# Kernel optimization log

Hardware: AMD Instinct MI355X
Metric: run time of the kernel (lower is better)

## Reference

```python
import jax, jax.numpy as jnp
import numpy as np

S = 3000    # number of candidate spans (rows of g_i)
P = 80000   # total (mention, antecedent) pairs
GI = 768    # gi_dim
DD = 20     # distance/genre/speaker embedding dim
HID = 150   # mlp hidden dim (fixed in source)
ORDER = 2   # N: one higher-order refinement pass


def setup_inputs() -> dict:
    key = jax.random.key(0)
    ks = jax.random.split(key, 18)
    gij = 3 * GI + 3 * DD
    g_i = jax.random.normal(ks[0], (S, GI), jnp.float32)
    mention_scores = jax.random.normal(ks[1], (S, 1), jnp.float32)
    # sorted segment ids: ragged antecedent counts per mention, grouped contiguously
    mention_ids = jnp.sort(jax.random.randint(ks[2], (P,), 0, S, dtype=jnp.int32))
    antecedent_ids = jax.random.randint(ks[3], (P,), 0, S, dtype=jnp.int32)
    dist_bins = jax.random.randint(ks[4], (P,), 0, 10, dtype=jnp.int32)
    genre_ids = jax.random.randint(ks[5], (P,), 0, 7, dtype=jnp.int32) + 1   # 1..7, 0 is padding_idx
    speaker_ids = jax.random.randint(ks[6], (P,), 0, 2, dtype=jnp.int32) + 1  # 1..2, 0 is padding_idx
    w = lambda k, shp: 0.02 * jax.random.normal(k, shp, jnp.float32)
    dist_emb = w(ks[7], (10, DD))
    genre_emb = w(ks[8], (8, DD)).at[0].set(0.0)     # padding_idx=0
    speaker_emb = w(ks[9], (3, DD)).at[0].set(0.0)   # padding_idx=0
    W1 = w(ks[10], (gij, HID)); b1 = jnp.zeros((HID,), jnp.float32)
    W2 = w(ks[11], (HID, HID)); b2 = jnp.zeros((HID,), jnp.float32)
    W3 = w(ks[12], (HID, 1)); b3 = jnp.zeros((1,), jnp.float32)
    Wf = w(ks[13], (2 * GI, 1)); bf = jnp.zeros((1,), jnp.float32)
    return {"g_i": g_i, "mention_scores": mention_scores, "mention_ids": mention_ids,
            "antecedent_ids": antecedent_ids, "dist_bins": dist_bins, "genre_ids": genre_ids,
            "speaker_ids": speaker_ids, "dist_emb": dist_emb, "genre_emb": genre_emb,
            "speaker_emb": speaker_emb, "W1": W1, "b1": b1, "W2": W2, "b2": b2,
            "W3": W3, "b3": b3, "Wf": Wf, "bf": bf}


def _mlp(x, W1, b1, W2, b2, W3, b3):
    h = jax.nn.relu(x @ W1 + b1)
    h = jax.nn.relu(h @ W2 + b2)
    return h @ W3 + b3


def reference(g_i, mention_scores, mention_ids, antecedent_ids, dist_bins, genre_ids,
              speaker_ids, dist_emb, genre_emb, speaker_emb, W1, b1, W2, b2, W3, b3, Wf, bf):
    phi = jnp.concatenate([dist_emb[dist_bins], genre_emb[genre_ids], speaker_emb[speaker_ids]], axis=1)  # [P,60]
    seg = dict(num_segments=S, indices_are_sorted=True)
    g = g_i
    scores = None
    for n in range(ORDER):
        i_g = g[mention_ids]                # [P,GI] gather
        j_g = g[antecedent_ids]             # [P,GI] gather
        pairs = jnp.concatenate([i_g, j_g, i_g * j_g, phi], axis=1)  # [P,gij]
        scores = _mlp(pairs, W1, b1, W2, b2, W3, b3)                 # [P,1]
        if n < ORDER - 1:
            # higher_order_refinement: ragged segment softmax + weighted scatter update
            s = scores[:, 0]
            seg_max = jax.ops.segment_max(s, mention_ids, **seg)
            safe_max = jnp.where(jnp.isfinite(seg_max), seg_max, 0.0)
            e = jnp.exp(s - safe_max[mention_ids])
            denom = jax.ops.segment_sum(e, mention_ids, **seg)
            attn = e / jnp.where(denom > 0, denom, 1.0)[mention_ids]
            weighted = jax.ops.segment_sum(attn[:, None] * j_g, mention_ids, **seg)  # [S,GI]
            counts = jax.ops.segment_sum(jnp.ones_like(s), mention_ids, **seg)
            f = jax.nn.sigmoid(jnp.concatenate([g, weighted], axis=1) @ Wf + bf)  # [S,1]
            # NOTE: faithful to the source bug: f * mention_id (the integer index), not f * mention_g
            ids_f = jnp.arange(S, dtype=g.dtype)[:, None]
            g_new = f * ids_f + (1.0 - f) * weighted
            g = jnp.where(counts[:, None] > 0, g_new, g)
    s_i = mention_scores[mention_ids]
    s_j = mention_scores[antecedent_ids]
    coref_scores = s_i + s_j + scores       # [P,1]
    # segment softmax with an extra epsilon (score 0) logit per mention
    c = coref_scores[:, 0]
    seg_max = jax.ops.segment_max(c, mention_ids, **seg)
    m = jnp.maximum(jnp.where(jnp.isfinite(seg_max), seg_max, 0.0), 0.0)  # include epsilon logit 0
    e = jnp.exp(c - m[mention_ids])
    denom = jax.ops.segment_sum(e, mention_ids, **seg) + jnp.exp(-m)
    pair_probs = e / denom[mention_ids]     # [P]
    eps_probs = jnp.exp(-m) / denom         # [S]
    return coref_scores, pair_probs, eps_probs
```

## Files before the change

### kernel.cpp

```cpp
#include <hip/hip_runtime.h>

#define GI   768
#define HID  150
#define HPAD 160
#define DDIM 20

typedef __attribute__((ext_vector_type(8))) short v8s;
typedef __attribute__((ext_vector_type(4))) float f32x4;
typedef __attribute__((ext_vector_type(16))) float f32x16;

#define MFMA(A, B, C)   __builtin_amdgcn_mfma_f32_32x32x16_bf16(A, B, C, 0, 0, 0)
#define MFMA16(A, B, C) __builtin_amdgcn_mfma_f32_16x16x32_bf16(A, B, C, 0, 0, 0)

__device__ __forceinline__ ushort bf16rn(float x) {
  unsigned u = __float_as_uint(x);
  return (ushort)((u + 0x7fffu + ((u >> 16) & 1u)) >> 16);
}
__device__ __forceinline__ void tsplit(float x, ushort& h, ushort& l) {
  unsigned u = __float_as_uint(x);
  h = (ushort)(u >> 16);
  float d = x - __uint_as_float(u & 0xffff0000u);
  l = (ushort)(__float_as_uint(d) >> 16);
}
__device__ __forceinline__ uint4 pack8(const ushort* v) {
  uint4 r;
  r.x = v[0] | ((unsigned)v[1] << 16); r.y = v[2] | ((unsigned)v[3] << 16);
  r.z = v[4] | ((unsigned)v[5] << 16); r.w = v[6] | ((unsigned)v[7] << 16);
  return r;
}
__device__ __forceinline__ v8s mk8(const ushort* v) {
  union { uint4 u; v8s s; } t;
  t.u = pack8(v);
  return t.s;
}

__global__ void seg_kernel(const int* __restrict__ mI, int* __restrict__ segs,
                           int P, int S) {
  int m = blockIdx.x * 256 + threadIdx.x;
  if (m > S) return;
  int lo = 0, hi = P;
  while (lo < hi) { int mid = (lo + hi) >> 1; if (mI[mid] < m) lo = mid + 1; else hi = mid; }
  segs[m] = lo;
}

__global__ void phi_kernel(const float* __restrict__ de, const float* __restrict__ ge,
                           const float* __restrict__ se, const float* __restrict__ W1,
                           float* __restrict__ phiW) {
  int idx = blockIdx.x * 256 + threadIdx.x;
  if (idx >= 21 * HPAD) return;
  int row = idx / HPAD, h = idx % HPAD;
  float v = 0.f;
  if (h < HID) {
    const float* emb; int off;
    if (row < 10)      { emb = de + row * DDIM;        off = 0; }
    else if (row < 18) { emb = ge + (row - 10) * DDIM; off = DDIM; }
    else               { emb = se + (row - 18) * DDIM; off = 2 * DDIM; }
    for (int k = 0; k < DDIM; ++k) v += emb[k] * W1[(3 * GI + off + k) * HID + h];
  }
  phiW[row * HPAD + h] = v;
}

#define NWC  (10 * 24 * 512)
#define NW16 (20 * 24 * 512)
#define NW2B (5 * 10 * 512)
__global__ void pad2_kernel(const float* __restrict__ W1, const float* __restrict__ W2,
                            const float* __restrict__ b1, const float* __restrict__ b2,
                            const float* __restrict__ W3,
                            ushort* __restrict__ WC, ushort* __restrict__ W16,
                            ushort* __restrict__ W2Bhi, ushort* __restrict__ W2Blo,
                            float* __restrict__ b1p, float2* __restrict__ b2w3) {
  int idx = blockIdx.x * 256 + threadIdx.x;
  if (idx < NWC) {
    int ct = idx / (24 * 512); int r1 = idx % (24 * 512);
    int s = r1 / 512; int r2 = r1 % 512;
    int l = r2 / 8, j = r2 % 8;
    int col = ct * 16 + (l & 15);
    int k = s * 32 + 8 * (l >> 4) + j;
    float x = (col < HID) ? W1[(size_t)(2 * GI + k) * HID + col] : 0.f;
    WC[idx] = bf16rn(x); return;
  }
  idx -= NWC;
  if (idx < NW16) {
    int ct = idx / (24 * 512); int r1 = idx % (24 * 512);
    int s = r1 / 512; int r2 = r1 % 512;
    int l = r2 / 8, j = r2 % 8;
    int col = ct * 16 + (l & 15);
    int k = s * 32 + 8 * (l >> 4) + j;
    int seg = col / HPAD, h = col % HPAD;
    float x = (h < HID) ? W1[(size_t)(seg * GI + k) * HID + h] : 0.f;
    W16[idx] = bf16rn(x); return;
  }
  idx -= NW16;
  if (idx < NW2B) {
    int rt = idx / (10 * 512); int r1 = idx % (10 * 512);
    int s = r1 / 512; int r2 = r1 % 512;
    int l = r2 / 8, j = r2 % 8;
    int h2 = rt * 32 + (l & 31);
    int k = s * 16 + 8 * (l >> 5) + j;
    float x = (k < HID && h2 < HID) ? W2[(size_t)k * HID + h2] : 0.f;
    ushort hh = bf16rn(x);
    float lo = x - __uint_as_float((unsigned)hh << 16);
    W2Bhi[idx] = hh; W2Blo[idx] = bf16rn(lo); return;
  }
  idx -= NW2B;
  if (idx < HPAD) { b1p[idx] = (idx < HID) ? b1[idx] : 0.f; return; }
  idx -= HPAD;
  if (idx < HPAD) {
    b2w3[idx] = make_float2((idx < HID) ? b2[idx] : 0.f, (idx < HID) ? W3[idx] : 0.f);
    return;
  }
}

__global__ __launch_bounds__(64, 4) void pre3_kernel(
    const float* __restrict__ g, const ushort* __restrict__ W16,
    float* __restrict__ pre, int S) {
  const int lane = threadIdx.x;
  const int ct = blockIdx.x;
  const int row0 = blockIdx.y * 16;
  int srow = row0 + (lane & 15); if (srow >= S) srow = S - 1;
  const float* gp = g + (size_t)srow * GI + 8 * (lane >> 4);
  const ushort* wp = W16 + ((size_t)ct * 24 * 64 + lane) * 8;

  f32x4 acc = {};
#pragma unroll 2
  for (int s = 0; s < 24; ++s) {
    const float4 a0 = *(const float4*)(gp + s * 32);
    const float4 a1 = *(const float4*)(gp + s * 32 + 4);
    const v8s bh = *(const v8s*)(wp + (size_t)s * 512);
    float xr[8] = {a0.x, a0.y, a0.z, a0.w, a1.x, a1.y, a1.z, a1.w};
    ushort hs[8], ls[8];
#pragma unroll
    for (int j = 0; j < 8; ++j) tsplit(xr[j], hs[j], ls[j]);
    const v8s ah = mk8(hs), al = mk8(ls);
    acc = MFMA16(ah, bh, acc);
    acc = MFMA16(al, bh, acc);
  }
  const int col = ct * 16 + (lane & 15);
#pragma unroll
  for (int r = 0; r < 4; ++r) {
    int sr = row0 + (lane >> 4) * 4 + r;
    if (sr < S) pre[(size_t)sr * 320 + col] = acc[r];
  }
}

__global__ __launch_bounds__(64, 4) void h1c_kernel(
    const float* __restrict__ g, const float* __restrict__ pre,
    const float* __restrict__ phiW, const ushort* __restrict__ WC,
    const float* __restrict__ b1p,
    const int* __restrict__ mI, const int* __restrict__ aI,
    const int* __restrict__ db, const int* __restrict__ ge, const int* __restrict__ sp,
    ushort* __restrict__ h1b, int P) {
  const int lane = threadIdx.x;
  const int lrow = lane & 15;
  const int kg = lane >> 4;
  const int p0 = blockIdx.x * 16;

  const int myp = p0 + lrow;
  const int iA = mI[myp], jA = aI[myp];
  const int rdL = db[myp], rgL = 10 + ge[myp], rsL = 18 + sp[myp];

  const float* gi = g + (size_t)iA * GI + 8 * kg;
  const float* gj = g + (size_t)jA * GI + 8 * kg;

  f32x4 acc[10];
  {
    f32x4 z = {};
#pragma unroll
    for (int c = 0; c < 10; ++c) acc[c] = z;
  }

#pragma unroll 2
  for (int s = 0; s < 24; ++s) {
    const int d0 = s * 32;
    const float4 a0 = *(const float4*)(gi + d0);
    const float4 a1 = *(const float4*)(gi + d0 + 4);
    const float4 b0 = *(const float4*)(gj + d0);
    const float4 b1v = *(const float4*)(gj + d0 + 4);
    float xr[8] = {a0.x * b0.x, a0.y * b0.y, a0.z * b0.z, a0.w * b0.w,
                   a1.x * b1v.x, a1.y * b1v.y, a1.z * b1v.z, a1.w * b1v.w};
    ushort hs[8], ls[8];
#pragma unroll
    for (int j = 0; j < 8; ++j) tsplit(xr[j], hs[j], ls[j]);
    const v8s ah = mk8(hs), al = mk8(ls);
#pragma unroll
    for (int c = 0; c < 10; ++c) {
      const v8s w = *(const v8s*)(WC + ((size_t)(c * 24 + s) * 64 + lane) * 8);
      acc[c] = MFMA16(ah, w, acc[c]);
      acc[c] = MFMA16(al, w, acc[c]);
    }
  }

#pragma unroll
  for (int r = 0; r < 4; ++r) {
    const int p = kg * 4 + r;
    const int pI = __shfl(iA, p);
    const int pJ = __shfl(jA, p);
    const int rd = __shfl(rdL, p), rg = __shfl(rgL, p), rs = __shfl(rsL, p);
    const float* preI = pre + (size_t)pI * 320;
    const float* preJ = pre + (size_t)pJ * 320 + 160;
    const size_t prow = (size_t)(p0 + p) * 160;
#pragma unroll
    for (int c = 0; c < 10; ++c) {
      const int col = c * 16 + lrow;
      float v = acc[c][r] + b1p[col] + preI[col] + preJ[col]
              + phiW[rd * HPAD + col] + phiW[rg * HPAD + col] + phiW[rs * HPAD + col];
      v = fmaxf(v, 0.f);
      h1b[prow + col] = bf16rn(v);
    }
  }
}

__global__ __launch_bounds__(64, 3) void score3_kernel(
    const ushort* __restrict__ h1b,
    const ushort* __restrict__ W2Bhi, const ushort* __restrict__ W2Blo,
    const float2* __restrict__ b2w3, const float* __restrict__ b3,
    float* __restrict__ sOut, int P) {
  const int lane = threadIdx.x;
  const int lcol = lane & 31, half = lane >> 5;
  const int p0 = blockIdx.x * 32;

  const ushort* hb = h1b + (size_t)(p0 + lcol) * 160 + 8 * half;

  f32x16 acc[5];
  {
    f32x16 z = {};
#pragma unroll
    for (int r = 0; r < 5; ++r) acc[r] = z;
  }

#pragma unroll 2
  for (int s = 0; s < 10; ++s) {
    const v8s b = *(const v8s*)(hb + s * 16);
#pragma unroll
    for (int r = 0; r < 5; ++r) {
      const size_t o = ((size_t)(r * 10 + s) * 64 + lane) * 8;
      const v8s ah = *(const v8s*)(W2Bhi + o);
      const v8s al = *(const v8s*)(W2Blo + o);
      acc[r] = MFMA(ah, b, acc[r]);
      acc[r] = MFMA(al, b, acc[r]);
    }
  }

  float part = 0.f;
#pragma unroll
  for (int r = 0; r < 5; ++r) {
#pragma unroll
    for (int q = 0; q < 16; ++q) {
      const int h2 = r * 32 + (q & 3) + 8 * (q >> 2) + 4 * half;
      const float2 bw = b2w3[h2];
      part += fmaxf(acc[r][q] + bw.x, 0.f) * bw.y;
    }
  }
  part += __shfl_xor(part, 32);
  if (lane < 32) sOut[p0 + lane] = part + b3[0];
}

__global__ void mid_kernel(const float* __restrict__ g, const float* __restrict__ s1,
                           const int* __restrict__ segs, const int* __restrict__ aI,
                           const float* __restrict__ Wf, const float* __restrict__ bf,
                           float* __restrict__ g2) {
  const int m = blockIdx.x;
  const int t = threadIdx.x;
  const int st = segs[m], en = segs[m + 1], n = en - st;
  if (n == 0) {
    for (int d = t; d < GI; d += 256) g2[m * GI + d] = g[m * GI + d];
    return;
  }
  __shared__ float red[256];
  __shared__ float wred[4][GI];
  float mx = -INFINITY;
  for (int p = st + t; p < en; p += 256) mx = fmaxf(mx, s1[p]);
  red[t] = mx; __syncthreads();
  for (int s = 128; s > 0; s >>= 1) { if (t < s) red[t] = fmaxf(red[t], red[t + s]); __syncthreads(); }
  mx = red[0]; __syncthreads();
  const int dg = t & 63, pg = t >> 6;
  float wv[12];
#pragma unroll
  for (int u = 0; u < 12; ++u) wv[u] = 0.f;
  float esum = 0.f;
  for (int p = st + pg; p < en; p += 4) {
    const float e = expf(s1[p] - mx);
    esum += e;
    const float* gj = g + (size_t)aI[p] * GI + dg;
#pragma unroll
    for (int u = 0; u < 12; ++u) wv[u] += e * gj[u * 64];
  }
  red[t] = (dg == 0) ? esum : 0.f; __syncthreads();
  for (int s = 128; s > 0; s >>= 1) { if (t < s) red[t] += red[t + s]; __syncthreads(); }
  const float denom = red[0]; __syncthreads();
#pragma unroll
  for (int u = 0; u < 12; ++u) wred[pg][dg + u * 64] = wv[u];
  __syncthreads();
  float part = 0.f;
  float wfin[3];
#pragma unroll
  for (int u = 0; u < 3; ++u) {
    const int d = t + u * 256;
    float wsv = (wred[0][d] + wred[1][d] + wred[2][d] + wred[3][d]) / denom;
    wfin[u] = wsv;
    part += g[(size_t)m * GI + d] * Wf[d] + wsv * Wf[GI + d];
  }
  red[t] = part; __syncthreads();
  for (int s = 128; s > 0; s >>= 1) { if (t < s) red[t] += red[t + s]; __syncthreads(); }
  const float f = 1.f / (1.f + expf(-(red[0] + bf[0])));
#pragma unroll
  for (int u = 0; u < 3; ++u) {
    const int d = t + u * 256;
    g2[(size_t)m * GI + d] = f * (float)m + (1.f - f) * wfin[u];
  }
}

__global__ void coref_kernel(const float* __restrict__ ms, const float* __restrict__ s2,
                             const int* __restrict__ mI, const int* __restrict__ aI,
                             float* __restrict__ out, int P) {
  int p = blockIdx.x * 256 + threadIdx.x;
  if (p >= P) return;
  out[p] = ms[mI[p]] + ms[aI[p]] + s2[p];
}

__global__ void final_kernel(const float* __restrict__ c, const int* __restrict__ segs,
                             float* __restrict__ pairP, float* __restrict__ epsP) {
  const int m = blockIdx.x;
  const int t = threadIdx.x;
  const int st = segs[m], en = segs[m + 1], n = en - st;
  __shared__ float red[256];
  float mx = -INFINITY;
  for (int p = st + t; p < en; p += 256) mx = fmaxf(mx, c[p]);
  red[t] = mx; __syncthreads();
  for (int s = 128; s > 0; s >>= 1) { if (t < s) red[t] = fmaxf(red[t], red[t + s]); __syncthreads(); }
  mx = red[0]; __syncthreads();
  const float m2 = (n > 0) ? fmaxf(mx, 0.f) : 0.f;
  float sm = 0.f;
  for (int p = st + t; p < en; p += 256) sm += expf(c[p] - m2);
  red[t] = sm; __syncthreads();
  for (int s = 128; s > 0; s >>= 1) { if (t < s) red[t] += red[t + s]; __syncthreads(); }
  const float denom = red[0] + expf(-m2);
  for (int p = st + t; p < en; p += 256) pairP[p] = expf(c[p] - m2) / denom;
  if (t == 0) epsP[m] = expf(-m2) / denom;
}

extern "C" void kernel_launch(void* const* d_in, const int* in_sizes, int n_in,
                              void* d_out, int out_size, void* d_ws, size_t ws_size,
                              hipStream_t stream) {
  const float* g_i  = (const float*)d_in[0];
  const float* ms   = (const float*)d_in[1];
  const int*   mI   = (const int*)d_in[2];
  const int*   aI   = (const int*)d_in[3];
  const int*   db   = (const int*)d_in[4];
  const int*   ge   = (const int*)d_in[5];
  const int*   sp   = (const int*)d_in[6];
  const float* de   = (const float*)d_in[7];
  const float* gemb = (const float*)d_in[8];
  const float* semb = (const float*)d_in[9];
  const float* W1   = (const float*)d_in[10];
  const float* b1   = (const float*)d_in[11];
  const float* W2   = (const float*)d_in[12];
  const float* b2   = (const float*)d_in[13];
  const float* W3   = (const float*)d_in[14];
  const float* b3   = (const float*)d_in[15];
  const float* Wf   = (const float*)d_in[16];
  const float* bf   = (const float*)d_in[17];

  const int S = in_sizes[0] / GI;
  const int P = in_sizes[2];
  float* out = (float*)d_out;

  char* ws = (char*)d_ws;
  size_t off = 0;
  auto take = [&](size_t bytes) -> char* {
    char* p = ws + off;
    off = (off + bytes + 15) & ~(size_t)15;
    return p;
  };
  int*    segs  = (int*)   take((size_t)(S + 1) * 4);
  float*  phiW  = (float*) take((size_t)21 * HPAD * 4);
  float*  pre   = (float*) take((size_t)S * 320 * 4);
  float*  g2    = (float*) take((size_t)S * GI * 4);
  float*  s1    = (float*) take((size_t)P * 4);
  float*  s2    = (float*) take((size_t)P * 4);
  ushort* WC    = (ushort*)take((size_t)NWC * 2);
  ushort* W16   = (ushort*)take((size_t)NW16 * 2);
  ushort* W2Bhi = (ushort*)take((size_t)NW2B * 2);
  ushort* W2Blo = (ushort*)take((size_t)NW2B * 2);
  float*  b1p   = (float*) take((size_t)HPAD * 4);
  float2* b2w3  = (float2*)take((size_t)HPAD * 8);
  ushort* h1b   = (ushort*)take((size_t)P * 160 * 2);

  const int gridSeg = (S + 1 + 255) / 256;
  const int gridPhi = (21 * HPAD + 255) / 256;
  const int padTot  = NWC + NW16 + NW2B + 2 * HPAD;
  const int gridPad = (padTot + 255) / 256;
  const dim3 gridPre(20, (S + 15) / 16);
  const int gridH   = P / 16;
  const int gridS3  = P / 32;
  const int gridCor = (P + 255) / 256;

  seg_kernel<<<gridSeg, 256, 0, stream>>>(mI, segs, P, S);
  phi_kernel<<<gridPhi, 256, 0, stream>>>(de, gemb, semb, W1, phiW);
  pad2_kernel<<<gridPad, 256, 0, stream>>>(W1, W2, b1, b2, W3, WC, W16,
                                           W2Bhi, W2Blo, b1p, b2w3);

  pre3_kernel<<<gridPre, 64, 0, stream>>>(g_i, W16, pre, S);
  h1c_kernel<<<gridH, 64, 0, stream>>>(g_i, pre, phiW, WC, b1p,
                                       mI, aI, db, ge, sp, h1b, P);
  score3_kernel<<<gridS3, 64, 0, stream>>>(h1b, W2Bhi, W2Blo, b2w3, b3, s1, P);
  mid_kernel<<<S, 256, 0, stream>>>(g_i, s1, segs, aI, Wf, bf, g2);

  pre3_kernel<<<gridPre, 64, 0, stream>>>(g2, W16, pre, S);
  h1c_kernel<<<gridH, 64, 0, stream>>>(g2, pre, phiW, WC, b1p,
                                       mI, aI, db, ge, sp, h1b, P);
  score3_kernel<<<gridS3, 64, 0, stream>>>(h1b, W2Bhi, W2Blo, b2w3, b3, s2, P);

  coref_kernel<<<gridCor, 256, 0, stream>>>(ms, s2, mI, aI, out, P);
  final_kernel<<<S, 256, 0, stream>>>(out, segs, out + P, out + 2 * (size_t)P);
}
```

Before: 488.1 us.

## Fuse second MLP layer into h1 kernel and use bf16 g for first pass

Merges the layer-2/score kernel into the layer-1 pair kernel: h1 is held in shared memory and fed to a 16x16 MFMA layer-2 with a repacked W2, which removes the P x 160 h1 round-trip through global memory and one launch per pass. The first refinement pass now reads a bf16 copy of g_i with a single-term product instead of the hi/lo split, roughly halving MFMA work and gather bytes there. The precomputed per-span projections are stored as bf16, and mid_kernel gathers from the bf16 g. These cuts trade away accuracy in the first-pass scores and attention, adding error relative to the reference.

```diff
diff --git a/kernel.cpp b/kernel.cpp
--- a/kernel.cpp
+++ b/kernel.cpp
@@ -7,14 +7,15 @@
 
 typedef __attribute__((ext_vector_type(8))) short v8s;
 typedef __attribute__((ext_vector_type(4))) float f32x4;
-typedef __attribute__((ext_vector_type(16))) float f32x16;
-
-#define MFMA(A, B, C)   __builtin_amdgcn_mfma_f32_32x32x16_bf16(A, B, C, 0, 0, 0)
+
 #define MFMA16(A, B, C) __builtin_amdgcn_mfma_f32_16x16x32_bf16(A, B, C, 0, 0, 0)
 
 __device__ __forceinline__ ushort bf16rn(float x) {
   unsigned u = __float_as_uint(x);
   return (ushort)((u + 0x7fffu + ((u >> 16) & 1u)) >> 16);
+}
+__device__ __forceinline__ float b2f(ushort u) {
+  return __uint_as_float((unsigned)u << 16);
 }
 __device__ __forceinline__ void tsplit(float x, ushort& h, ushort& l) {
   unsigned u = __float_as_uint(x);
@@ -60,14 +61,23 @@
   phiW[row * HPAD + h] = v;
 }
 
+__global__ void g2b_kernel(const float* __restrict__ g, ushort* __restrict__ gb, int n4) {
+  int i = blockIdx.x * 256 + threadIdx.x;
+  if (i >= n4) return;
+  const float4 v = *(const float4*)(g + 4 * (size_t)i);
+  ushort4 o;
+  o.x = bf16rn(v.x); o.y = bf16rn(v.y); o.z = bf16rn(v.z); o.w = bf16rn(v.w);
+  *(ushort4*)(gb + 4 * (size_t)i) = o;
+}
+
 #define NWC  (10 * 24 * 512)
 #define NW16 (20 * 24 * 512)
-#define NW2B (5 * 10 * 512)
+#define NW2C (10 * 5 * 512)
 __global__ void pad2_kernel(const float* __restrict__ W1, const float* __restrict__ W2,
                             const float* __restrict__ b1, const float* __restrict__ b2,
                             const float* __restrict__ W3,
                             ushort* __restrict__ WC, ushort* __restrict__ W16,
-                            ushort* __restrict__ W2Bhi, ushort* __restrict__ W2Blo,
+                            ushort* __restrict__ W2Chi, ushort* __restrict__ W2Clo,
                             float* __restrict__ b1p, float2* __restrict__ b2w3) {
   int idx = blockIdx.x * 256 + threadIdx.x;
   if (idx < NWC) {
@@ -91,18 +101,18 @@
     W16[idx] = bf16rn(x); return;
   }
   idx -= NW16;
-  if (idx < NW2B) {
-    int rt = idx / (10 * 512); int r1 = idx % (10 * 512);
+  if (idx < NW2C) {
+    int ct = idx / (5 * 512); int r1 = idx % (5 * 512);
     int s = r1 / 512; int r2 = r1 % 512;
     int l = r2 / 8, j = r2 % 8;
-    int h2 = rt * 32 + (l & 31);
-    int k = s * 16 + 8 * (l >> 5) + j;
-    float x = (k < HID && h2 < HID) ? W2[(size_t)k * HID + h2] : 0.f;
+    int col = ct * 16 + (l & 15);
+    int k = s * 32 + 8 * (l >> 4) + j;
+    float x = (k < HID && col < HID) ? W2[(size_t)k * HID + col] : 0.f;
     ushort hh = bf16rn(x);
     float lo = x - __uint_as_float((unsigned)hh << 16);
-    W2Bhi[idx] = hh; W2Blo[idx] = bf16rn(lo); return;
-  }
-  idx -= NW2B;
+    W2Chi[idx] = hh; W2Clo[idx] = bf16rn(lo); return;
+  }
+  idx -= NW2C;
   if (idx < HPAD) { b1p[idx] = (idx < HID) ? b1[idx] : 0.f; return; }
   idx -= HPAD;
   if (idx < HPAD) {
@@ -113,7 +123,7 @@
 
 __global__ __launch_bounds__(64, 4) void pre3_kernel(
     const float* __restrict__ g, const ushort* __restrict__ W16,
-    float* __restrict__ pre, int S) {
+    ushort* __restrict__ preb, int S) {
   const int lane = threadIdx.x;
   const int ct = blockIdx.x;
   const int row0 = blockIdx.y * 16;
@@ -139,29 +149,30 @@
 #pragma unroll
   for (int r = 0; r < 4; ++r) {
     int sr = row0 + (lane >> 4) * 4 + r;
-    if (sr < S) pre[(size_t)sr * 320 + col] = acc[r];
-  }
-}
-
-__global__ __launch_bounds__(64, 4) void h1c_kernel(
-    const float* __restrict__ g, const float* __restrict__ pre,
-    const float* __restrict__ phiW, const ushort* __restrict__ WC,
-    const float* __restrict__ b1p,
+    if (sr < S) preb[(size_t)sr * 320 + col] = bf16rn(acc[r]);
+  }
+}
+
+template<bool BF16G>
+__global__ __launch_bounds__(64, 4) void h1s_kernel(
+    const float* __restrict__ g, const ushort* __restrict__ gb,
+    const ushort* __restrict__ preb, const float* __restrict__ phiW,
+    const ushort* __restrict__ WC,
+    const ushort* __restrict__ W2Chi, const ushort* __restrict__ W2Clo,
+    const float* __restrict__ b1p, const float2* __restrict__ b2w3,
+    const float* __restrict__ b3,
     const int* __restrict__ mI, const int* __restrict__ aI,
-    const int* __restrict__ db, const int* __restrict__ ge, const int* __restrict__ sp,
-    ushort* __restrict__ h1b, int P) {
+    const int* __restrict__ db, const int* __restrict__ ge,
+    const int* __restrict__ sp,
+    float* __restrict__ sOut, int P) {
+  __shared__ ushort h1L[16 * 160];
   const int lane = threadIdx.x;
-  const int lrow = lane & 15;
-  const int kg = lane >> 4;
+  const int lrow = lane & 15, kg = lane >> 4;
   const int p0 = blockIdx.x * 16;
-
   const int myp = p0 + lrow;
   const int iA = mI[myp], jA = aI[myp];
   const int rdL = db[myp], rgL = 10 + ge[myp], rsL = 18 + sp[myp];
 
-  const float* gi = g + (size_t)iA * GI + 8 * kg;
-  const float* gj = g + (size_t)jA * GI + 8 * kg;
-
   f32x4 acc[10];
   {
     f32x4 z = {};
@@ -169,24 +180,47 @@
     for (int c = 0; c < 10; ++c) acc[c] = z;
   }
 
+  if constexpr (BF16G) {
+    const ushort* gbi = gb + (size_t)iA * GI + 8 * kg;
+    const ushort* gbj = gb + (size_t)jA * GI + 8 * kg;
 #pragma unroll 2
-  for (int s = 0; s < 24; ++s) {
-    const int d0 = s * 32;
-    const float4 a0 = *(const float4*)(gi + d0);
-    const float4 a1 = *(const float4*)(gi + d0 + 4);
-    const float4 b0 = *(const float4*)(gj + d0);
-    const float4 b1v = *(const float4*)(gj + d0 + 4);
-    float xr[8] = {a0.x * b0.x, a0.y * b0.y, a0.z * b0.z, a0.w * b0.w,
-                   a1.x * b1v.x, a1.y * b1v.y, a1.z * b1v.z, a1.w * b1v.w};
-    ushort hs[8], ls[8];
-#pragma unroll
-    for (int j = 0; j < 8; ++j) tsplit(xr[j], hs[j], ls[j]);
-    const v8s ah = mk8(hs), al = mk8(ls);
-#pragma unroll
-    for (int c = 0; c < 10; ++c) {
-      const v8s w = *(const v8s*)(WC + ((size_t)(c * 24 + s) * 64 + lane) * 8);
-      acc[c] = MFMA16(ah, w, acc[c]);
-      acc[c] = MFMA16(al, w, acc[c]);
+    for (int s = 0; s < 24; ++s) {
+      const int d0 = s * 32;
+      const v8s ai = *(const v8s*)(gbi + d0);
+      const v8s aj = *(const v8s*)(gbj + d0);
+      ushort pr[8];
+#pragma unroll
+      for (int j = 0; j < 8; ++j)
+        pr[j] = bf16rn(b2f((ushort)ai[j]) * b2f((ushort)aj[j]));
+      const v8s ap = mk8(pr);
+#pragma unroll
+      for (int c = 0; c < 10; ++c) {
+        const v8s w = *(const v8s*)(WC + ((size_t)(c * 24 + s) * 64 + lane) * 8);
+        acc[c] = MFMA16(ap, w, acc[c]);
+      }
+    }
+  } else {
+    const float* gi = g + (size_t)iA * GI + 8 * kg;
+    const float* gj = g + (size_t)jA * GI + 8 * kg;
+#pragma unroll 2
+    for (int s = 0; s < 24; ++s) {
+      const int d0 = s * 32;
+      const float4 a0 = *(const float4*)(gi + d0);
+      const float4 a1 = *(const float4*)(gi + d0 + 4);
+      const float4 b0 = *(const float4*)(gj + d0);
+      const float4 b1v = *(const float4*)(gj + d0 + 4);
+      float xr[8] = {a0.x * b0.x, a0.y * b0.y, a0.z * b0.z, a0.w * b0.w,
+                     a1.x * b1v.x, a1.y * b1v.y, a1.z * b1v.z, a1.w * b1v.w};
+      ushort hs[8], ls[8];
+#pragma unroll
+      for (int j = 0; j < 8; ++j) tsplit(xr[j], hs[j], ls[j]);
+      const v8s ah = mk8(hs), al = mk8(ls);
+#pragma unroll
+      for (int c = 0; c < 10; ++c) {
+        const v8s w = *(const v8s*)(WC + ((size_t)(c * 24 + s) * 64 + lane) * 8);
+        acc[c] = MFMA16(ah, w, acc[c]);
+        acc[c] = MFMA16(al, w, acc[c]);
+      }
     }
   }
 
@@ -196,66 +230,59 @@
     const int pI = __shfl(iA, p);
     const int pJ = __shfl(jA, p);
     const int rd = __shfl(rdL, p), rg = __shfl(rgL, p), rs = __shfl(rsL, p);
-    const float* preI = pre + (size_t)pI * 320;
-    const float* preJ = pre + (size_t)pJ * 320 + 160;
-    const size_t prow = (size_t)(p0 + p) * 160;
+    const ushort* prI = preb + (size_t)pI * 320;
+    const ushort* prJ = preb + (size_t)pJ * 320 + 160;
 #pragma unroll
     for (int c = 0; c < 10; ++c) {
       const int col = c * 16 + lrow;
-      float v = acc[c][r] + b1p[col] + preI[col] + preJ[col]
+      float v = acc[c][r] + b1p[col] + b2f(prI[col]) + b2f(prJ[col])
               + phiW[rd * HPAD + col] + phiW[rg * HPAD + col] + phiW[rs * HPAD + col];
       v = fmaxf(v, 0.f);
-      h1b[prow + col] = bf16rn(v);
+      h1L[p * 160 + col] = bf16rn(v);
     }
   }
-}
-
-__global__ __launch_bounds__(64, 3) void score3_kernel(
-    const ushort* __restrict__ h1b,
-    const ushort* __restrict__ W2Bhi, const ushort* __restrict__ W2Blo,
-    const float2* __restrict__ b2w3, const float* __restrict__ b3,
-    float* __restrict__ sOut, int P) {
-  const int lane = threadIdx.x;
-  const int lcol = lane & 31, half = lane >> 5;
-  const int p0 = blockIdx.x * 32;
-
-  const ushort* hb = h1b + (size_t)(p0 + lcol) * 160 + 8 * half;
-
-  f32x16 acc[5];
+  __syncthreads();
+
+  f32x4 acc2[10];
   {
-    f32x16 z = {};
-#pragma unroll
-    for (int r = 0; r < 5; ++r) acc[r] = z;
-  }
-
-#pragma unroll 2
-  for (int s = 0; s < 10; ++s) {
-    const v8s b = *(const v8s*)(hb + s * 16);
-#pragma unroll
-    for (int r = 0; r < 5; ++r) {
-      const size_t o = ((size_t)(r * 10 + s) * 64 + lane) * 8;
-      const v8s ah = *(const v8s*)(W2Bhi + o);
-      const v8s al = *(const v8s*)(W2Blo + o);
-      acc[r] = MFMA(ah, b, acc[r]);
-      acc[r] = MFMA(al, b, acc[r]);
+    f32x4 z = {};
+#pragma unroll
+    for (int ct = 0; ct < 10; ++ct) acc2[ct] = z;
+  }
+#pragma unroll
+  for (int s = 0; s < 5; ++s) {
+    const v8s a = *(const v8s*)(&h1L[lrow * 160 + s * 32 + 8 * kg]);
+#pragma unroll
+    for (int ct = 0; ct < 10; ++ct) {
+      const size_t o = ((size_t)(ct * 5 + s) * 64 + lane) * 8;
+      const v8s wh = *(const v8s*)(W2Chi + o);
+      const v8s wl = *(const v8s*)(W2Clo + o);
+      acc2[ct] = MFMA16(a, wh, acc2[ct]);
+      acc2[ct] = MFMA16(a, wl, acc2[ct]);
     }
   }
-
-  float part = 0.f;
-#pragma unroll
-  for (int r = 0; r < 5; ++r) {
-#pragma unroll
-    for (int q = 0; q < 16; ++q) {
-      const int h2 = r * 32 + (q & 3) + 8 * (q >> 2) + 4 * half;
-      const float2 bw = b2w3[h2];
-      part += fmaxf(acc[r][q] + bw.x, 0.f) * bw.y;
-    }
-  }
-  part += __shfl_xor(part, 32);
-  if (lane < 32) sOut[p0 + lane] = part + b3[0];
-}
-
-__global__ void mid_kernel(const float* __restrict__ g, const float* __restrict__ s1,
+  float part[4] = {0.f, 0.f, 0.f, 0.f};
+#pragma unroll
+  for (int ct = 0; ct < 10; ++ct) {
+    const float2 bw = b2w3[ct * 16 + lrow];
+#pragma unroll
+    for (int r = 0; r < 4; ++r)
+      part[r] += fmaxf(acc2[ct][r] + bw.x, 0.f) * bw.y;
+  }
+#pragma unroll
+  for (int m = 1; m < 16; m <<= 1) {
+#pragma unroll
+    for (int r = 0; r < 4; ++r) part[r] += __shfl_xor(part[r], m, 16);
+  }
+  if (lrow == 0) {
+    const float bb = b3[0];
+#pragma unroll
+    for (int r = 0; r < 4; ++r) sOut[p0 + kg * 4 + r] = part[r] + bb;
+  }
+}
+
+__global__ void mid_kernel(const float* __restrict__ g, const ushort* __restrict__ gb,
+                           const float* __restrict__ s1,
                            const int* __restrict__ segs, const int* __restrict__ aI,
                            const float* __restrict__ Wf, const float* __restrict__ bf,
                            float* __restrict__ g2) {
@@ -281,9 +308,9 @@
   for (int p = st + pg; p < en; p += 4) {
     const float e = expf(s1[p] - mx);
     esum += e;
-    const float* gj = g + (size_t)aI[p] * GI + dg;
-#pragma unroll
-    for (int u = 0; u < 12; ++u) wv[u] += e * gj[u * 64];
+    const ushort* gj = gb + (size_t)aI[p] * GI + dg;
+#pragma unroll
+    for (int u = 0; u < 12; ++u) wv[u] += e * b2f(gj[u * 64]);
   }
   red[t] = (dg == 0) ? esum : 0.f; __syncthreads();
   for (int s = 128; s > 0; s >>= 1) { if (t < s) red[t] += red[t + s]; __syncthreads(); }
@@ -374,42 +401,42 @@
   };
   int*    segs  = (int*)   take((size_t)(S + 1) * 4);
   float*  phiW  = (float*) take((size_t)21 * HPAD * 4);
-  float*  pre   = (float*) take((size_t)S * 320 * 4);
+  ushort* preb  = (ushort*)take((size_t)S * 320 * 2);
   float*  g2    = (float*) take((size_t)S * GI * 4);
   float*  s1    = (float*) take((size_t)P * 4);
   float*  s2    = (float*) take((size_t)P * 4);
+  ushort* Gb    = (ushort*)take((size_t)S * GI * 2);
   ushort* WC    = (ushort*)take((size_t)NWC * 2);
   ushort* W16   = (ushort*)take((size_t)NW16 * 2);
-  ushort* W2Bhi = (ushort*)take((size_t)NW2B * 2);
-  ushort* W2Blo = (ushort*)take((size_t)NW2B * 2);
+  ushort* W2Chi = (ushort*)take((size_t)NW2C * 2);
+  ushort* W2Clo = (ushort*)take((size_t)NW2C * 2);
   float*  b1p   = (float*) take((size_t)HPAD * 4);
   float2* b2w3  = (float2*)take((size_t)HPAD * 8);
-  ushort* h1b   = (ushort*)take((size_t)P * 160 * 2);
 
   const int gridSeg = (S + 1 + 255) / 256;
   const int gridPhi = (21 * HPAD + 255) / 256;
-  const int padTot  = NWC + NW16 + NW2B + 2 * HPAD;
+  const int padTot  = NWC + NW16 + NW2C + 2 * HPAD;
   const int gridPad = (padTot + 255) / 256;
+  const int n4      = S * GI / 4;
+  const int gridGb  = (n4 + 255) / 256;
   const dim3 gridPre(20, (S + 15) / 16);
   const int gridH   = P / 16;
-  const int gridS3  = P / 32;
   const int gridCor = (P + 255) / 256;
 
   seg_kernel<<<gridSeg, 256, 0, stream>>>(mI, segs, P, S);
   phi_kernel<<<gridPhi, 256, 0, stream>>>(de, gemb, semb, W1, phiW);
   pad2_kernel<<<gridPad, 256, 0, stream>>>(W1, W2, b1, b2, W3, WC, W16,
-                                           W2Bhi, W2Blo, b1p, b2w3);
-
-  pre3_kernel<<<gridPre, 64, 0, stream>>>(g_i, W16, pre, S);
-  h1c_kernel<<<gridH, 64, 0, stream>>>(g_i, pre, phiW, WC, b1p,
-                                       mI, aI, db, ge, sp, h1b, P);
-  score3_kernel<<<gridS3, 64, 0, stream>>>(h1b, W2Bhi, W2Blo, b2w3, b3, s1, P);
-  mid_kernel<<<S, 256, 0, stream>>>(g_i, s1, segs, aI, Wf, bf, g2);
-
-  pre3_kernel<<<gridPre, 64, 0, stream>>>(g2, W16, pre, S);
-  h1c_kernel<<<gridH, 64, 0, stream>>>(g2, pre, phiW, WC, b1p,
-                                       mI, aI, db, ge, sp, h1b, P);
-  score3_kernel<<<gridS3, 64, 0, stream>>>(h1b, W2Bhi, W2Blo, b2w3, b3, s2, P);
+                                           W2Chi, W2Clo, b1p, b2w3);
+  g2b_kernel<<<gridGb, 256, 0, stream>>>(g_i, Gb, n4);
+
+  pre3_kernel<<<gridPre, 64, 0, stream>>>(g_i, W16, preb, S);
+  h1s_kernel<true><<<gridH, 64, 0, stream>>>(g_i, Gb, preb, phiW, WC, W2Chi, W2Clo,
+                                             b1p, b2w3, b3, mI, aI, db, ge, sp, s1, P);
+  mid_kernel<<<S, 256, 0, stream>>>(g_i, Gb, s1, segs, aI, Wf, bf, g2);
+
+  pre3_kernel<<<gridPre, 64, 0, stream>>>(g2, W16, preb, S);
+  h1s_kernel<false><<<gridH, 64, 0, stream>>>(g2, Gb, preb, phiW, WC, W2Chi, W2Clo,
+                                              b1p, b2w3, b3, mI, aI, db, ge, sp, s2, P);
 
   coref_kernel<<<gridCor, 256, 0, stream>>>(ms, s2, mI, aI, out, P);
   final_kernel<<<S, 256, 0, stream>>>(out, segs, out + P, out + 2 * (size_t)P);
```

After: 447.8 us. 8.3% less time.
